# Performance work log

Measured on AMD Instinct MI355X. Metric: run time of the kernel, lower is better.

Reference implementation:

```python
import jax, jax.numpy as jnp
import numpy as np

HEADS = 16
LN_EPS = 1e-5

def setup_inputs() -> dict:
    key = jax.random.key(0)
    ks = jax.random.split(key, 8)
    B, S, NT = 4, 1024, 1024
    sc = 1.0 / np.sqrt(NT)
    return {
        "x": jax.random.normal(ks[0], (B, S, NT), dtype=jnp.float32),
        "Wq": jax.random.normal(ks[1], (NT, NT), dtype=jnp.float32) * sc,
        "bq": jax.random.normal(ks[2], (NT,), dtype=jnp.float32) * 0.02,
        "Wk": jax.random.normal(ks[3], (NT, NT), dtype=jnp.float32) * sc,
        "bk": jax.random.normal(ks[4], (NT,), dtype=jnp.float32) * 0.02,
        "Wv": jax.random.normal(ks[5], (NT, NT), dtype=jnp.float32) * sc,
        "bv": jax.random.normal(ks[6], (NT,), dtype=jnp.float32) * 0.02,
        "gamma": jnp.ones((NT,), dtype=jnp.float32),
        "beta": jnp.zeros((NT,), dtype=jnp.float32),
    }

def reference(x, Wq, bq, Wk, bk, Wv, bv, gamma, beta):
    B, S, nt = x.shape
    heads = HEADS
    dph = nt // heads
    # torch nn.Linear: y = x @ W.T + b
    q = x @ Wq.T + bq
    k = x @ Wk.T + bk
    v = x @ Wv.T + bv
    # torch .view(B*heads, -1, dph) is a row-major reshape (interleaved split)
    q = q.reshape(B * heads, -1, dph)
    k = k.reshape(B * heads, -1, dph)
    v = v.reshape(B * heads, -1, dph)
    # scaled scores; scale uses last dim of the score matrix (== seq len here)
    att = jnp.einsum('bid,bjd->bij', q, k)
    scale = att.shape[-1] ** (-0.5)
    att = jax.nn.softmax(jax.nn.relu(att * scale), axis=-1)
    # dropout in eval mode -> identity
    at_sum_sum = att.sum(axis=1).reshape(B, heads, -1)  # [B, heads, S]
    context = jnp.einsum('bij,bjd->bid', att, v).reshape(B, -1, nt)
    h = x + context
    mu = h.mean(axis=-1, keepdims=True)
    var = h.var(axis=-1, keepdims=True)
    out = (h - mu) * jax.lax.rsqrt(var + LN_EPS) * gamma + beta
    return out, at_sum_sum
```

## Files before the change

kernel.cpp:

```cpp
#include <hip/hip_runtime.h>
#include <hip/hip_bf16.h>
#include <cstdint>
#include <cstddef>


typedef short short8 __attribute__((ext_vector_type(8)));
typedef short short4v __attribute__((ext_vector_type(4)));
typedef float f32x4 __attribute__((ext_vector_type(4)));

#define MFMA32(a, b, c) __builtin_amdgcn_mfma_f32_16x16x32_bf16(a, b, c, 0, 0, 0)
#define MFMA16x16(a, b, c) __builtin_amdgcn_mfma_f32_16x16x16bf16_1k(a, b, c, 0, 0, 0)
#define ATT_SCALE 0.03125f

__device__ __forceinline__ short f2bf(float f) {
  union { float f; uint32_t u; } x; x.f = f;
  uint32_t u = x.u + 0x7fffu + ((x.u >> 16) & 1u);
  return (short)(u >> 16);
}

__device__ __forceinline__ uint32_t pk_bf16_trunc(float lo, float hi) {
  return __builtin_amdgcn_perm(__float_as_uint(hi), __float_as_uint(lo),
                               0x07060302u);
}

#define GLDS16(gp, lp)                                                        \
  __builtin_amdgcn_global_load_lds(                                           \
      (const __attribute__((address_space(1))) void*)(gp),                    \
      (__attribute__((address_space(3))) void*)(lp), 16, 0, 0)
#define GLDS4(gp, lp)                                                         \
  __builtin_amdgcn_global_load_lds(                                           \
      (const __attribute__((address_space(1))) void*)(gp),                    \
      (__attribute__((address_space(3))) void*)(lp), 4, 0, 0)

__global__ __launch_bounds__(256) void convert_kernel(
    const float* __restrict__ x, const float* __restrict__ wq,
    const float* __restrict__ wk, const float* __restrict__ wv,
    short* __restrict__ xb, short* __restrict__ wb,
    float* __restrict__ out2) {
  if (blockIdx.x >= 7168) {
    const int idx = (blockIdx.x - 7168) * 256 + threadIdx.x;
    *(f32x4*)(out2 + (size_t)idx * 4) = (f32x4){0.f, 0.f, 0.f, 0.f};
    return;
  }
  const long XN = 4L * 1024 * 1024, WN = 1024L * 1024;
  long e = (long)(blockIdx.x * blockDim.x + threadIdx.x) * 4;
  const float* src; short* dst;
  if (e < XN)               { src = x  + e;                dst = xb + e; }
  else if (e < XN + WN)     { src = wq + (e - XN);         dst = wb + (e - XN); }
  else if (e < XN + 2 * WN) { src = wk + (e - XN - WN);    dst = wb + (e - XN); }
  else                      { src = wv + (e - XN - 2*WN);  dst = wb + (e - XN); }
  f32x4 v = *(const f32x4*)src;
  short4v o;
  o[0] = f2bf(v[0]); o[1] = f2bf(v[1]); o[2] = f2bf(v[2]); o[3] = f2bf(v[3]);
  *(short4v*)dst = o;
}

__global__ __launch_bounds__(256, 3) void qkv_gemm(
    const short* __restrict__ xb, const short* __restrict__ wb,
    const float* __restrict__ bq, const float* __restrict__ bk,
    const float* __restrict__ bv, short* __restrict__ qb,
    short* __restrict__ kb, short* __restrict__ vtp) {
  __shared__ short As[128 * 64];
  __shared__ short Bs[128 * 64];
  const int tid = threadIdx.x;
  const int lane = tid & 63;
  const int lm = lane & 15, quad = lane >> 4;
  const int wave = tid >> 6, wy = wave >> 1, wx = wave & 1;
  const int f = blockIdx.x + (blockIdx.y << 3);
  const int r8 = f & 7, s = f >> 3;
  const int m0 = (((r8 >> 1) << 3) + (s & 7)) * 128;
  const int n0 = (((r8 & 1) << 2) + (s >> 3)) * 128;
  const int z = blockIdx.z;
  const short* w = wb + (size_t)z * (1024 * 1024);
  const float* bias = (z == 0) ? bq : (z == 1) ? bk : bv;
  const float scl = (z == 0) ? ATT_SCALE : 1.0f;

  const int srow = tid >> 3;
  const int schk = (tid & 7) ^ (srow & 7);
  const short* gA = xb + (size_t)(m0 + srow) * 1024 + schk * 8;
  const short* gB = w  + (size_t)(n0 + srow) * 1024 + schk * 8;
  short* lA = As + tid * 8;
  short* lB = Bs + tid * 8;

  f32x4 acc[4][4];
#pragma unroll
  for (int i = 0; i < 4; i++)
#pragma unroll
    for (int j = 0; j < 4; j++) acc[i][j] = (f32x4){0.f, 0.f, 0.f, 0.f};

  for (int k0 = 0; k0 < 1024; k0 += 64) {
#pragma unroll
    for (int q = 0; q < 4; q++) {
      GLDS16(gA + k0 + q * 32 * 1024, lA + q * 2048);
      GLDS16(gB + k0 + q * 32 * 1024, lB + q * 2048);
    }
    __syncthreads();
#pragma unroll
    for (int ks = 0; ks < 2; ks++) {
      const int ck = (((ks << 2) + quad) ^ (lm & 7)) * 8;
      short8 a[4], b[4];
#pragma unroll
      for (int t = 0; t < 4; t++) {
        a[t] = *(const short8*)(As + (wy * 64 + t * 16 + lm) * 64 + ck);
        b[t] = *(const short8*)(Bs + (wx * 64 + t * 16 + lm) * 64 + ck);
      }
#pragma unroll
      for (int mt = 0; mt < 4; mt++)
#pragma unroll
        for (int nt = 0; nt < 4; nt++)
          acc[mt][nt] = MFMA32(a[mt], b[nt], acc[mt][nt]);
    }
    __syncthreads();
  }
  if (z == 2) {
#pragma unroll
    for (int nt = 0; nt < 4; nt++) {
      const int n = n0 + wx * 64 + nt * 16 + lm;
      const float bn = bias[n];
      const size_t nbase = (size_t)((n >> 4) & 3) * 16384 +
                           (size_t)((((n >> 8) & 3) * 16 + (n & 15)) * 4 +
                                    ((n >> 6) & 3));
#pragma unroll
      for (int mt = 0; mt < 4; mt++) {
#pragma unroll
        for (int r = 0; r < 4; r++) {
          const int m = m0 + wy * 64 + mt * 16 + quad * 4 + r;
          vtp[(size_t)(m >> 6) * 65536 + nbase + (size_t)(m & 63) * 256] =
              f2bf(acc[mt][nt][r] + bn);
        }
      }
    }
  } else {
    short* out = (z == 0) ? qb : kb;
#pragma unroll
    for (int nt = 0; nt < 4; nt++) {
      const int n = n0 + wx * 64 + nt * 16 + lm;
      const float bn = bias[n];
#pragma unroll
      for (int mt = 0; mt < 4; mt++) {
        const int mb = m0 + wy * 64 + mt * 16 + quad * 4;
#pragma unroll
        for (int r = 0; r < 4; r++)
          out[(size_t)(mb + r) * 1024 + n] = f2bf((acc[mt][nt][r] + bn) * scl);
      }
    }
  }
}

__global__ __launch_bounds__(256, 2) void attn_kernel(
    const short* __restrict__ qb, const short* __restrict__ kb,
    const short* __restrict__ vtp, const float* __restrict__ x,
    const float* __restrict__ gamma, const float* __restrict__ beta,
    float* __restrict__ out1, float* __restrict__ rvW) {
  __shared__ short Ks[3][64 * 64];
  __shared__ short Vs[3][4 * 4 * 256];

  const int tid = threadIdx.x;
  const int lane = tid & 63, wave = tid >> 6;
  const int lm = lane & 15, quad = lane >> 4;
  const int bid = blockIdx.x;
  const int h = ((bid >> 6) << 3) + (bid & 7);
  const int bb = (bid >> 3) & 7;
  const short* Qh = qb + (size_t)h * 65536;
  const short* Kh = kb + (size_t)h * 65536;
  const short* Vp = vtp + (size_t)h * 65536;
  const int i0 = bb * 128 + wave * 32;

  const short8 qA0 = *(const short8*)(Qh + (size_t)(i0 + lm) * 64 + quad * 8);
  const short8 qA1 = *(const short8*)(Qh + (size_t)(i0 + lm) * 64 + 32 + quad * 8);
  const short8 qB0 = *(const short8*)(Qh + (size_t)(i0 + 16 + lm) * 64 + quad * 8);
  const short8 qB1 = *(const short8*)(Qh + (size_t)(i0 + 16 + lm) * 64 + 32 + quad * 8);

  const int c0 = tid, c1 = tid + 256;
  const short* gK0 = Kh + (size_t)(c0 >> 3) * 64 + ((c0 & 7) ^ ((c0 >> 3) & 7)) * 8;
  const short* gK1 = Kh + (size_t)(c1 >> 3) * 64 + ((c1 & 7) ^ ((c1 >> 3) & 7)) * 8;
  const short* gV0 = Vp + (c0 >> 7) * 16384 + ((c0 >> 5) & 3) * 256 + (c0 & 31) * 8;
  const short* gV1 = Vp + (c1 >> 7) * 16384 + ((c1 >> 5) & 3) * 256 + (c1 & 31) * 8;
  const int lK0 = c0 * 8, lK1 = c1 * 8;

#define ATTN_STAGE(c, buf)                                                    \
  do {                                                                        \
    const int ko_ = ((c) & 15) * 4096, vo_ = ((c) & 15) * 1024;               \
    GLDS16(gK0 + ko_, &Ks[buf][0] + lK0);                                     \
    GLDS16(gK1 + ko_, &Ks[buf][0] + lK1);                                     \
    GLDS16(gV0 + vo_, &Vs[buf][0] + lK0);                                     \
    GLDS16(gV1 + vo_, &Vs[buf][0] + lK1);                                     \
  } while (0)

  f32x4 accA[4], accB[4];
#pragma unroll
  for (int t = 0; t < 4; t++) {
    accA[t] = (f32x4){0.f, 0.f, 0.f, 0.f};
    accB[t] = (f32x4){0.f, 0.f, 0.f, 0.f};
  }
  float dsA[4] = {0.f, 0.f, 0.f, 0.f};
  float dsB[4] = {0.f, 0.f, 0.f, 0.f};

  const int swz0 = (quad ^ (lm & 7)) * 8;
  const int swz1 = ((quad + 4) ^ (lm & 7)) * 8;

  ATTN_STAGE(0, 0);
  ATTN_STAGE(1, 1);

  for (int ch = 0; ch < 16; ch++) {
    const int b = ch % 3, bs = (ch + 2) % 3;
    asm volatile("s_waitcnt vmcnt(4)" ::: "memory");
    __builtin_amdgcn_s_barrier();
    __builtin_amdgcn_s_setprio(1);
#pragma unroll
    for (int jj = 0; jj < 4; jj++) {
      const short* krow = &Ks[b][(jj * 16 + lm) * 64];
      const short8 kf0 = *(const short8*)(krow + swz0);
      const short8 kf1 = *(const short8*)(krow + swz1);
      f32x4 zA = {0.f, 0.f, 0.f, 0.f};
      zA = MFMA32(kf0, qA0, zA);
      zA = MFMA32(kf1, qA1, zA);
      f32x4 zB = {0.f, 0.f, 0.f, 0.f};
      zB = MFMA32(kf0, qB0, zB);
      zB = MFMA32(kf1, qB1, zB);
      float pA[4], pB[4];
#pragma unroll
      for (int r = 0; r < 4; r++) {
        pA[r] = __expf(fmaxf(zA[r], 0.f));
        dsA[r] += pA[r];
        pB[r] = __expf(fmaxf(zB[r], 0.f));
        dsB[r] += pB[r];
      }
      union { uint32_t u[2]; short4v s; } puA, puB;
      puA.u[0] = pk_bf16_trunc(pA[0], pA[1]);
      puA.u[1] = pk_bf16_trunc(pA[2], pA[3]);
      puB.u[0] = pk_bf16_trunc(pB[0], pB[1]);
      puB.u[1] = pk_bf16_trunc(pB[2], pB[3]);
      const short* vbase = &Vs[b][jj * 256 + lane * 4];
#pragma unroll
      for (int dt = 0; dt < 4; dt++) {
        const short4v vtf = *(const short4v*)(vbase + dt * 1024);
        accA[dt] = MFMA16x16(vtf, puA.s, accA[dt]);
        accB[dt] = MFMA16x16(vtf, puB.s, accB[dt]);
      }
    }
    __builtin_amdgcn_s_setprio(0);
    if (ch < 15) ATTN_STAGE(ch + 2, bs);
  }
  asm volatile("s_waitcnt vmcnt(0)" ::: "memory");

  float tA = (dsA[0] + dsA[1]) + (dsA[2] + dsA[3]);
  tA += __shfl_xor(tA, 16);
  tA += __shfl_xor(tA, 32);
  float tB = (dsB[0] + dsB[1]) + (dsB[2] + dsB[3]);
  tB += __shfl_xor(tB, 16);
  tB += __shfl_xor(tB, 32);
  const float rvA = 1.f / tA;
  const float rvB = 1.f / tB;
  if (lane < 16) {
    rvW[h * 1024 + i0 + lm] = rvA;
    rvW[h * 1024 + i0 + 16 + lm] = rvB;
  }

  const int mA = h * 64 + bb * 8 + wave * 2;
  const int nb = lm * 64 + quad * 4;
#pragma unroll
  for (int tile = 0; tile < 2; tile++) {
    const int m = mA + tile;
    const f32x4* accT = tile ? accB : accA;
    const float rv = tile ? rvB : rvA;
    const float* xr = x + (size_t)m * 1024;
    float hv[4][4], s1 = 0.f, s2 = 0.f;
#pragma unroll
    for (int dt = 0; dt < 4; dt++) {
      f32x4 xv = *(const f32x4*)(xr + nb + dt * 16);
#pragma unroll
      for (int r = 0; r < 4; r++) {
        const float v = xv[r] + accT[dt][r] * rv;
        hv[dt][r] = v; s1 += v; s2 += v * v;
      }
    }
#pragma unroll
    for (int mk = 1; mk < 64; mk <<= 1) {
      s1 += __shfl_xor(s1, mk);
      s2 += __shfl_xor(s2, mk);
    }
    const float mu = s1 * (1.f / 1024.f);
    const float var = s2 * (1.f / 1024.f) - mu * mu;
    const float rstd = rsqrtf(var + 1e-5f);
    float* orow = out1 + (size_t)m * 1024;
#pragma unroll
    for (int dt = 0; dt < 4; dt++) {
      f32x4 gv = *(const f32x4*)(gamma + nb + dt * 16);
      f32x4 bv2 = *(const f32x4*)(beta + nb + dt * 16);
      f32x4 ov;
#pragma unroll
      for (int r = 0; r < 4; r++)
        ov[r] = (hv[dt][r] - mu) * rstd * gv[r] + bv2[r];
      *(f32x4*)(orow + nb + dt * 16) = ov;
    }
  }
}

__global__ __launch_bounds__(256, 4) void colsum_kernel(
    const short* __restrict__ qb, const short* __restrict__ kb,
    const float* __restrict__ rvW, float* __restrict__ out2) {
  __shared__ short Qs[3][64 * 64];
  __shared__ float rvS[3][64];

  const int tid = threadIdx.x;
  const int lane = tid & 63, wave = tid >> 6;
  const int lm = lane & 15, quad = lane >> 4;
  const int bid = blockIdx.x;
  const int h = ((bid >> 7) << 3) + (bid & 7);
  const int jb = (bid >> 3) & 7;
  const int ih = (bid >> 6) & 1;
  const int cb = ih * 8;
  const int j0 = jb * 128 + wave * 32;
  const short* Qh = qb + (size_t)h * 65536;
  const short* Kh = kb + (size_t)h * 65536;
  const float* rvh = rvW + h * 1024;

  const short* krA = Kh + (size_t)(j0 + lm) * 64 + quad * 8;
  const short8 kA0 = *(const short8*)krA;
  const short8 kA1 = *(const short8*)(krA + 32);
  const short* krB = Kh + (size_t)(j0 + 16 + lm) * 64 + quad * 8;
  const short8 kB0 = *(const short8*)krB;
  const short8 kB1 = *(const short8*)(krB + 32);

  const int c0 = tid, c1 = tid + 256;
  const short* gQ0 = Qh + (size_t)(c0 >> 3) * 64 + ((c0 & 7) ^ ((c0 >> 3) & 7)) * 8;
  const short* gQ1 = Qh + (size_t)(c1 >> 3) * 64 + ((c1 & 7) ^ ((c1 >> 3) & 7)) * 8;
  const int lQ0 = c0 * 8, lQ1 = c1 * 8;

#define CS_STAGE(c, buf)                                                      \
  do {                                                                        \
    const int qo_ = ((c) & 15) * 4096;                                        \
    GLDS16(gQ0 + qo_, &Qs[buf][0] + lQ0);                                     \
    GLDS16(gQ1 + qo_, &Qs[buf][0] + lQ1);                                     \
    GLDS4(rvh + ((c) & 15) * 64 + lane, &rvS[buf][0]);                        \
  } while (0)

  const int swz0 = (quad ^ (lm & 7)) * 8;
  const int swz1 = ((quad + 4) ^ (lm & 7)) * 8;

  f32x4 csA = {0.f, 0.f, 0.f, 0.f};
  f32x4 csB = {0.f, 0.f, 0.f, 0.f};

  CS_STAGE(cb, 0);
  CS_STAGE(cb + 1, 1);

  for (int ch = 0; ch < 8; ch++) {
    const int b = ch % 3, bs = (ch + 2) % 3;
    asm volatile("s_waitcnt vmcnt(3)" ::: "memory");
    __builtin_amdgcn_s_barrier();
    __builtin_amdgcn_s_setprio(1);
#pragma unroll
    for (int ii = 0; ii < 4; ii++) {
      const short* qrow = &Qs[b][(ii * 16 + lm) * 64];
      const short8 qf0 = *(const short8*)(qrow + swz0);
      const short8 qf1 = *(const short8*)(qrow + swz1);
      f32x4 zA = {0.f, 0.f, 0.f, 0.f};
      zA = MFMA32(kA0, qf0, zA);
      zA = MFMA32(kA1, qf1, zA);
      f32x4 zB = {0.f, 0.f, 0.f, 0.f};
      zB = MFMA32(kB0, qf0, zB);
      zB = MFMA32(kB1, qf1, zB);
      const float rvv = rvS[b][ii * 16 + lm];
#pragma unroll
      for (int r = 0; r < 4; r++) {
        csA[r] += __expf(fmaxf(zA[r], 0.f)) * rvv;
        csB[r] += __expf(fmaxf(zB[r], 0.f)) * rvv;
      }
    }
    __builtin_amdgcn_s_setprio(0);
    if (ch < 7) CS_STAGE((cb + ch + 2) & 15, bs);
  }
  asm volatile("s_waitcnt vmcnt(0)" ::: "memory");

#pragma unroll
  for (int mk = 1; mk < 16; mk <<= 1)
#pragma unroll
    for (int r = 0; r < 4; r++) {
      csA[r] += __shfl_xor(csA[r], mk);
      csB[r] += __shfl_xor(csB[r], mk);
    }
  if (lm == 0) {
    float* pA = out2 + h * 1024 + j0 + quad * 4;
    float* pB = pA + 16;
#pragma unroll
    for (int r = 0; r < 4; r++) {
      atomicAdd(pA + r, csA[r]);
      atomicAdd(pB + r, csB[r]);
    }
  }
}

extern "C" void kernel_launch(void* const* d_in, const int* in_sizes, int n_in,
                              void* d_out, int out_size, void* d_ws, size_t ws_size,
                              hipStream_t stream) {
  const float* x  = (const float*)d_in[0];
  const float* Wq = (const float*)d_in[1];
  const float* bq = (const float*)d_in[2];
  const float* Wk = (const float*)d_in[3];
  const float* bk = (const float*)d_in[4];
  const float* Wv = (const float*)d_in[5];
  const float* bv = (const float*)d_in[6];
  const float* gamma = (const float*)d_in[7];
  const float* beta  = (const float*)d_in[8];

  float* out1 = (float*)d_out;
  float* out2 = out1 + 4L * 1024 * 1024;

  short* xb = (short*)d_ws;
  short* wb = xb + 4L * 1024 * 1024;
  short* qb = wb + 3L * 1024 * 1024;
  short* kb = qb + 4L * 1024 * 1024;
  short* vtp = kb + 4L * 1024 * 1024;
  float* rvW = (float*)wb;

  convert_kernel<<<7232, 256, 0, stream>>>(x, Wq, Wk, Wv, xb, wb, out2);
  qkv_gemm<<<dim3(8, 32, 3), 256, 0, stream>>>(xb, wb, bq, bk, bv, qb, kb, vtp);
  attn_kernel<<<512, 256, 0, stream>>>(qb, kb, vtp, x, gamma, beta, out1, rvW);
  colsum_kernel<<<1024, 256, 0, stream>>>(qb, kb, rvW, out2);
}
```

Measured before the change: 165.3 us.

## Fold log2e into Q scale, read V and colsum Q directly from global

Folds log2(e) into the Q projection scale so both softmax kernels can call the hardware exp2 instruction instead of __expf. In the attention kernel, V fragments are no longer staged through LDS; each lane loads them straight from global memory. In the colsum kernel, the LDS staging and barriers for Q and the row values are removed in favour of direct global loads. The aim is to cut LDS traffic, barriers and the extra multiply in exp, at the risk of exposing global load latency inside the MFMA loop.

```diff
diff --git a/kernel.cpp b/kernel.cpp
--- a/kernel.cpp
+++ b/kernel.cpp
@@ -10,7 +10,7 @@
 
 #define MFMA32(a, b, c) __builtin_amdgcn_mfma_f32_16x16x32_bf16(a, b, c, 0, 0, 0)
 #define MFMA16x16(a, b, c) __builtin_amdgcn_mfma_f32_16x16x16bf16_1k(a, b, c, 0, 0, 0)
-#define ATT_SCALE 0.03125f
+#define QSCALE 0.045084220027780106f
 
 __device__ __forceinline__ short f2bf(float f) {
   union { float f; uint32_t u; } x; x.f = f;
@@ -27,10 +27,6 @@
   __builtin_amdgcn_global_load_lds(                                           \
       (const __attribute__((address_space(1))) void*)(gp),                    \
       (__attribute__((address_space(3))) void*)(lp), 16, 0, 0)
-#define GLDS4(gp, lp)                                                         \
-  __builtin_amdgcn_global_load_lds(                                           \
-      (const __attribute__((address_space(1))) void*)(gp),                    \
-      (__attribute__((address_space(3))) void*)(lp), 4, 0, 0)
 
 __global__ __launch_bounds__(256) void convert_kernel(
     const float* __restrict__ x, const float* __restrict__ wq,
@@ -73,7 +69,7 @@
   const int z = blockIdx.z;
   const short* w = wb + (size_t)z * (1024 * 1024);
   const float* bias = (z == 0) ? bq : (z == 1) ? bk : bv;
-  const float scl = (z == 0) ? ATT_SCALE : 1.0f;
+  const float scl = (z == 0) ? QSCALE : 1.0f;
 
   const int srow = tid >> 3;
   const int schk = (tid & 7) ^ (srow & 7);
@@ -153,7 +149,6 @@
     const float* __restrict__ gamma, const float* __restrict__ beta,
     float* __restrict__ out1, float* __restrict__ rvW) {
   __shared__ short Ks[3][64 * 64];
-  __shared__ short Vs[3][4 * 4 * 256];
 
   const int tid = threadIdx.x;
   const int lane = tid & 63, wave = tid >> 6;
@@ -174,17 +169,14 @@
   const int c0 = tid, c1 = tid + 256;
   const short* gK0 = Kh + (size_t)(c0 >> 3) * 64 + ((c0 & 7) ^ ((c0 >> 3) & 7)) * 8;
   const short* gK1 = Kh + (size_t)(c1 >> 3) * 64 + ((c1 & 7) ^ ((c1 >> 3) & 7)) * 8;
-  const short* gV0 = Vp + (c0 >> 7) * 16384 + ((c0 >> 5) & 3) * 256 + (c0 & 31) * 8;
-  const short* gV1 = Vp + (c1 >> 7) * 16384 + ((c1 >> 5) & 3) * 256 + (c1 & 31) * 8;
   const int lK0 = c0 * 8, lK1 = c1 * 8;
+  const short* vl = Vp + lane * 4;
 
 #define ATTN_STAGE(c, buf)                                                    \
   do {                                                                        \
-    const int ko_ = ((c) & 15) * 4096, vo_ = ((c) & 15) * 1024;               \
+    const int ko_ = ((c) & 15) * 4096;                                        \
     GLDS16(gK0 + ko_, &Ks[buf][0] + lK0);                                     \
     GLDS16(gK1 + ko_, &Ks[buf][0] + lK1);                                     \
-    GLDS16(gV0 + vo_, &Vs[buf][0] + lK0);                                     \
-    GLDS16(gV1 + vo_, &Vs[buf][0] + lK1);                                     \
   } while (0)
 
   f32x4 accA[4], accB[4];
@@ -204,9 +196,10 @@
 
   for (int ch = 0; ch < 16; ch++) {
     const int b = ch % 3, bs = (ch + 2) % 3;
-    asm volatile("s_waitcnt vmcnt(4)" ::: "memory");
+    asm volatile("s_waitcnt vmcnt(2)" ::: "memory");
     __builtin_amdgcn_s_barrier();
     __builtin_amdgcn_s_setprio(1);
+    const short* vc = vl + ch * 1024;
 #pragma unroll
     for (int jj = 0; jj < 4; jj++) {
       const short* krow = &Ks[b][(jj * 16 + lm) * 64];
@@ -221,9 +214,9 @@
       float pA[4], pB[4];
 #pragma unroll
       for (int r = 0; r < 4; r++) {
-        pA[r] = __expf(fmaxf(zA[r], 0.f));
+        pA[r] = __builtin_amdgcn_exp2f(fmaxf(zA[r], 0.f));
         dsA[r] += pA[r];
-        pB[r] = __expf(fmaxf(zB[r], 0.f));
+        pB[r] = __builtin_amdgcn_exp2f(fmaxf(zB[r], 0.f));
         dsB[r] += pB[r];
       }
       union { uint32_t u[2]; short4v s; } puA, puB;
@@ -231,10 +224,10 @@
       puA.u[1] = pk_bf16_trunc(pA[2], pA[3]);
       puB.u[0] = pk_bf16_trunc(pB[0], pB[1]);
       puB.u[1] = pk_bf16_trunc(pB[2], pB[3]);
-      const short* vbase = &Vs[b][jj * 256 + lane * 4];
+      const short* vj = vc + jj * 256;
 #pragma unroll
       for (int dt = 0; dt < 4; dt++) {
-        const short4v vtf = *(const short4v*)(vbase + dt * 1024);
+        const short4v vtf = *(const short4v*)(vj + dt * 16384);
         accA[dt] = MFMA16x16(vtf, puA.s, accA[dt]);
         accB[dt] = MFMA16x16(vtf, puB.s, accB[dt]);
       }
@@ -300,9 +293,6 @@
 __global__ __launch_bounds__(256, 4) void colsum_kernel(
     const short* __restrict__ qb, const short* __restrict__ kb,
     const float* __restrict__ rvW, float* __restrict__ out2) {
-  __shared__ short Qs[3][64 * 64];
-  __shared__ float rvS[3][64];
-
   const int tid = threadIdx.x;
   const int lane = tid & 63, wave = tid >> 6;
   const int lm = lane & 15, quad = lane >> 4;
@@ -310,11 +300,10 @@
   const int h = ((bid >> 7) << 3) + (bid & 7);
   const int jb = (bid >> 3) & 7;
   const int ih = (bid >> 6) & 1;
-  const int cb = ih * 8;
   const int j0 = jb * 128 + wave * 32;
-  const short* Qh = qb + (size_t)h * 65536;
+  const short* Qh = qb + (size_t)h * 65536 + (size_t)ih * 32768;
   const short* Kh = kb + (size_t)h * 65536;
-  const float* rvh = rvW + h * 1024;
+  const float* rvh = rvW + h * 1024 + ih * 512;
 
   const short* krA = Kh + (size_t)(j0 + lm) * 64 + quad * 8;
   const short8 kA0 = *(const short8*)krA;
@@ -323,55 +312,33 @@
   const short8 kB0 = *(const short8*)krB;
   const short8 kB1 = *(const short8*)(krB + 32);
 
-  const int c0 = tid, c1 = tid + 256;
-  const short* gQ0 = Qh + (size_t)(c0 >> 3) * 64 + ((c0 & 7) ^ ((c0 >> 3) & 7)) * 8;
-  const short* gQ1 = Qh + (size_t)(c1 >> 3) * 64 + ((c1 & 7) ^ ((c1 >> 3) & 7)) * 8;
-  const int lQ0 = c0 * 8, lQ1 = c1 * 8;
-
-#define CS_STAGE(c, buf)                                                      \
-  do {                                                                        \
-    const int qo_ = ((c) & 15) * 4096;                                        \
-    GLDS16(gQ0 + qo_, &Qs[buf][0] + lQ0);                                     \
-    GLDS16(gQ1 + qo_, &Qs[buf][0] + lQ1);                                     \
-    GLDS4(rvh + ((c) & 15) * 64 + lane, &rvS[buf][0]);                        \
-  } while (0)
-
-  const int swz0 = (quad ^ (lm & 7)) * 8;
-  const int swz1 = ((quad + 4) ^ (lm & 7)) * 8;
-
   f32x4 csA = {0.f, 0.f, 0.f, 0.f};
   f32x4 csB = {0.f, 0.f, 0.f, 0.f};
 
-  CS_STAGE(cb, 0);
-  CS_STAGE(cb + 1, 1);
-
   for (int ch = 0; ch < 8; ch++) {
-    const int b = ch % 3, bs = (ch + 2) % 3;
-    asm volatile("s_waitcnt vmcnt(3)" ::: "memory");
-    __builtin_amdgcn_s_barrier();
+    const short* qc = Qh + ch * 4096 + (size_t)lm * 64 + quad * 8;
+    const float* rvc = rvh + ch * 64 + lm;
     __builtin_amdgcn_s_setprio(1);
 #pragma unroll
     for (int ii = 0; ii < 4; ii++) {
-      const short* qrow = &Qs[b][(ii * 16 + lm) * 64];
-      const short8 qf0 = *(const short8*)(qrow + swz0);
-      const short8 qf1 = *(const short8*)(qrow + swz1);
+      const short* qrow = qc + ii * 1024;
+      const short8 qf0 = *(const short8*)qrow;
+      const short8 qf1 = *(const short8*)(qrow + 32);
       f32x4 zA = {0.f, 0.f, 0.f, 0.f};
       zA = MFMA32(kA0, qf0, zA);
       zA = MFMA32(kA1, qf1, zA);
       f32x4 zB = {0.f, 0.f, 0.f, 0.f};
       zB = MFMA32(kB0, qf0, zB);
       zB = MFMA32(kB1, qf1, zB);
-      const float rvv = rvS[b][ii * 16 + lm];
+      const float rvv = rvc[ii * 16];
 #pragma unroll
       for (int r = 0; r < 4; r++) {
-        csA[r] += __expf(fmaxf(zA[r], 0.f)) * rvv;
-        csB[r] += __expf(fmaxf(zB[r], 0.f)) * rvv;
+        csA[r] += __builtin_amdgcn_exp2f(fmaxf(zA[r], 0.f)) * rvv;
+        csB[r] += __builtin_amdgcn_exp2f(fmaxf(zB[r], 0.f)) * rvv;
       }
     }
     __builtin_amdgcn_s_setprio(0);
-    if (ch < 7) CS_STAGE((cb + ch + 2) & 15, bs);
-  }
-  asm volatile("s_waitcnt vmcnt(0)" ::: "memory");
+  }
 
 #pragma unroll
   for (int mk = 1; mk < 16; mk <<= 1)
```

Result: slower. 181.3 us (+9.7%).

## Halve attention rows per block, double grid, fold log2e into Q scale

Applied to the files above, without the earlier changes.

The attention kernel now gives each wave 16 query rows instead of 32 and launches twice as many blocks. LDS staging drops from triple to double buffering, and launch bounds rise to 4 blocks per CU for more occupancy. The Q projection scale is multiplied by log2(e) so both attention and colsum can use the native exp2 instead of __expf. The cost is twice the K/V traffic per query row and a full vmcnt(0) wait each chunk, which removes some load/compute overlap.

```diff
diff --git a/kernel.cpp b/kernel.cpp
--- a/kernel.cpp
+++ b/kernel.cpp
@@ -10,7 +10,7 @@
 
 #define MFMA32(a, b, c) __builtin_amdgcn_mfma_f32_16x16x32_bf16(a, b, c, 0, 0, 0)
 #define MFMA16x16(a, b, c) __builtin_amdgcn_mfma_f32_16x16x16bf16_1k(a, b, c, 0, 0, 0)
-#define ATT_SCALE 0.03125f
+#define QSCALE 0.045084220027780106f
 
 __device__ __forceinline__ short f2bf(float f) {
   union { float f; uint32_t u; } x; x.f = f;
@@ -73,7 +73,7 @@
   const int z = blockIdx.z;
   const short* w = wb + (size_t)z * (1024 * 1024);
   const float* bias = (z == 0) ? bq : (z == 1) ? bk : bv;
-  const float scl = (z == 0) ? ATT_SCALE : 1.0f;
+  const float scl = (z == 0) ? QSCALE : 1.0f;
 
   const int srow = tid >> 3;
   const int schk = (tid & 7) ^ (srow & 7);
@@ -147,29 +147,27 @@
   }
 }
 
-__global__ __launch_bounds__(256, 2) void attn_kernel(
+__global__ __launch_bounds__(256, 4) void attn_kernel(
     const short* __restrict__ qb, const short* __restrict__ kb,
     const short* __restrict__ vtp, const float* __restrict__ x,
     const float* __restrict__ gamma, const float* __restrict__ beta,
     float* __restrict__ out1, float* __restrict__ rvW) {
-  __shared__ short Ks[3][64 * 64];
-  __shared__ short Vs[3][4 * 4 * 256];
+  __shared__ short Ks[2][64 * 64];
+  __shared__ short Vs[2][4 * 4 * 256];
 
   const int tid = threadIdx.x;
   const int lane = tid & 63, wave = tid >> 6;
   const int lm = lane & 15, quad = lane >> 4;
   const int bid = blockIdx.x;
-  const int h = ((bid >> 6) << 3) + (bid & 7);
-  const int bb = (bid >> 3) & 7;
+  const int h = ((bid >> 7) << 3) + (bid & 7);
+  const int blk = (bid >> 3) & 15;
   const short* Qh = qb + (size_t)h * 65536;
   const short* Kh = kb + (size_t)h * 65536;
   const short* Vp = vtp + (size_t)h * 65536;
-  const int i0 = bb * 128 + wave * 32;
+  const int i0 = blk * 64 + wave * 16;
 
   const short8 qA0 = *(const short8*)(Qh + (size_t)(i0 + lm) * 64 + quad * 8);
   const short8 qA1 = *(const short8*)(Qh + (size_t)(i0 + lm) * 64 + 32 + quad * 8);
-  const short8 qB0 = *(const short8*)(Qh + (size_t)(i0 + 16 + lm) * 64 + quad * 8);
-  const short8 qB1 = *(const short8*)(Qh + (size_t)(i0 + 16 + lm) * 64 + 32 + quad * 8);
 
   const int c0 = tid, c1 = tid + 256;
   const short* gK0 = Kh + (size_t)(c0 >> 3) * 64 + ((c0 & 7) ^ ((c0 >> 3) & 7)) * 8;
@@ -180,32 +178,28 @@
 
 #define ATTN_STAGE(c, buf)                                                    \
   do {                                                                        \
-    const int ko_ = ((c) & 15) * 4096, vo_ = ((c) & 15) * 1024;               \
+    const int ko_ = (c) * 4096, vo_ = (c) * 1024;                             \
     GLDS16(gK0 + ko_, &Ks[buf][0] + lK0);                                     \
     GLDS16(gK1 + ko_, &Ks[buf][0] + lK1);                                     \
     GLDS16(gV0 + vo_, &Vs[buf][0] + lK0);                                     \
     GLDS16(gV1 + vo_, &Vs[buf][0] + lK1);                                     \
   } while (0)
 
-  f32x4 accA[4], accB[4];
-#pragma unroll
-  for (int t = 0; t < 4; t++) {
-    accA[t] = (f32x4){0.f, 0.f, 0.f, 0.f};
-    accB[t] = (f32x4){0.f, 0.f, 0.f, 0.f};
-  }
+  f32x4 accA[4];
+#pragma unroll
+  for (int t = 0; t < 4; t++) accA[t] = (f32x4){0.f, 0.f, 0.f, 0.f};
   float dsA[4] = {0.f, 0.f, 0.f, 0.f};
-  float dsB[4] = {0.f, 0.f, 0.f, 0.f};
 
   const int swz0 = (quad ^ (lm & 7)) * 8;
   const int swz1 = ((quad + 4) ^ (lm & 7)) * 8;
 
   ATTN_STAGE(0, 0);
-  ATTN_STAGE(1, 1);
 
   for (int ch = 0; ch < 16; ch++) {
-    const int b = ch % 3, bs = (ch + 2) % 3;
-    asm volatile("s_waitcnt vmcnt(4)" ::: "memory");
+    const int b = ch & 1;
+    asm volatile("s_waitcnt vmcnt(0)" ::: "memory");
     __builtin_amdgcn_s_barrier();
+    if (ch < 15) ATTN_STAGE(ch + 1, b ^ 1);
     __builtin_amdgcn_s_setprio(1);
 #pragma unroll
     for (int jj = 0; jj < 4; jj++) {
@@ -215,85 +209,62 @@
       f32x4 zA = {0.f, 0.f, 0.f, 0.f};
       zA = MFMA32(kf0, qA0, zA);
       zA = MFMA32(kf1, qA1, zA);
-      f32x4 zB = {0.f, 0.f, 0.f, 0.f};
-      zB = MFMA32(kf0, qB0, zB);
-      zB = MFMA32(kf1, qB1, zB);
-      float pA[4], pB[4];
+      float pA[4];
 #pragma unroll
       for (int r = 0; r < 4; r++) {
-        pA[r] = __expf(fmaxf(zA[r], 0.f));
+        pA[r] = __builtin_amdgcn_exp2f(fmaxf(zA[r], 0.f));
         dsA[r] += pA[r];
-        pB[r] = __expf(fmaxf(zB[r], 0.f));
-        dsB[r] += pB[r];
-      }
-      union { uint32_t u[2]; short4v s; } puA, puB;
+      }
+      union { uint32_t u[2]; short4v s; } puA;
       puA.u[0] = pk_bf16_trunc(pA[0], pA[1]);
       puA.u[1] = pk_bf16_trunc(pA[2], pA[3]);
-      puB.u[0] = pk_bf16_trunc(pB[0], pB[1]);
-      puB.u[1] = pk_bf16_trunc(pB[2], pB[3]);
       const short* vbase = &Vs[b][jj * 256 + lane * 4];
 #pragma unroll
       for (int dt = 0; dt < 4; dt++) {
         const short4v vtf = *(const short4v*)(vbase + dt * 1024);
         accA[dt] = MFMA16x16(vtf, puA.s, accA[dt]);
-        accB[dt] = MFMA16x16(vtf, puB.s, accB[dt]);
       }
     }
     __builtin_amdgcn_s_setprio(0);
-    if (ch < 15) ATTN_STAGE(ch + 2, bs);
-  }
-  asm volatile("s_waitcnt vmcnt(0)" ::: "memory");
+  }
 
   float tA = (dsA[0] + dsA[1]) + (dsA[2] + dsA[3]);
   tA += __shfl_xor(tA, 16);
   tA += __shfl_xor(tA, 32);
-  float tB = (dsB[0] + dsB[1]) + (dsB[2] + dsB[3]);
-  tB += __shfl_xor(tB, 16);
-  tB += __shfl_xor(tB, 32);
   const float rvA = 1.f / tA;
-  const float rvB = 1.f / tB;
-  if (lane < 16) {
-    rvW[h * 1024 + i0 + lm] = rvA;
-    rvW[h * 1024 + i0 + 16 + lm] = rvB;
-  }
-
-  const int mA = h * 64 + bb * 8 + wave * 2;
+  if (lane < 16) rvW[h * 1024 + i0 + lm] = rvA;
+
+  const int m = h * 64 + blk * 4 + wave;
   const int nb = lm * 64 + quad * 4;
-#pragma unroll
-  for (int tile = 0; tile < 2; tile++) {
-    const int m = mA + tile;
-    const f32x4* accT = tile ? accB : accA;
-    const float rv = tile ? rvB : rvA;
-    const float* xr = x + (size_t)m * 1024;
-    float hv[4][4], s1 = 0.f, s2 = 0.f;
-#pragma unroll
-    for (int dt = 0; dt < 4; dt++) {
-      f32x4 xv = *(const f32x4*)(xr + nb + dt * 16);
-#pragma unroll
-      for (int r = 0; r < 4; r++) {
-        const float v = xv[r] + accT[dt][r] * rv;
-        hv[dt][r] = v; s1 += v; s2 += v * v;
-      }
-    }
-#pragma unroll
-    for (int mk = 1; mk < 64; mk <<= 1) {
-      s1 += __shfl_xor(s1, mk);
-      s2 += __shfl_xor(s2, mk);
-    }
-    const float mu = s1 * (1.f / 1024.f);
-    const float var = s2 * (1.f / 1024.f) - mu * mu;
-    const float rstd = rsqrtf(var + 1e-5f);
-    float* orow = out1 + (size_t)m * 1024;
-#pragma unroll
-    for (int dt = 0; dt < 4; dt++) {
-      f32x4 gv = *(const f32x4*)(gamma + nb + dt * 16);
-      f32x4 bv2 = *(const f32x4*)(beta + nb + dt * 16);
-      f32x4 ov;
-#pragma unroll
-      for (int r = 0; r < 4; r++)
-        ov[r] = (hv[dt][r] - mu) * rstd * gv[r] + bv2[r];
-      *(f32x4*)(orow + nb + dt * 16) = ov;
-    }
+  const float* xr = x + (size_t)m * 1024;
+  float hv[4][4], s1 = 0.f, s2 = 0.f;
+#pragma unroll
+  for (int dt = 0; dt < 4; dt++) {
+    f32x4 xv = *(const f32x4*)(xr + nb + dt * 16);
+#pragma unroll
+    for (int r = 0; r < 4; r++) {
+      const float v = xv[r] + accA[dt][r] * rvA;
+      hv[dt][r] = v; s1 += v; s2 += v * v;
+    }
+  }
+#pragma unroll
+  for (int mk = 1; mk < 64; mk <<= 1) {
+    s1 += __shfl_xor(s1, mk);
+    s2 += __shfl_xor(s2, mk);
+  }
+  const float mu = s1 * (1.f / 1024.f);
+  const float var = s2 * (1.f / 1024.f) - mu * mu;
+  const float rstd = rsqrtf(var + 1e-5f);
+  float* orow = out1 + (size_t)m * 1024;
+#pragma unroll
+  for (int dt = 0; dt < 4; dt++) {
+    f32x4 gv = *(const f32x4*)(gamma + nb + dt * 16);
+    f32x4 bv2 = *(const f32x4*)(beta + nb + dt * 16);
+    f32x4 ov;
+#pragma unroll
+    for (int r = 0; r < 4; r++)
+      ov[r] = (hv[dt][r] - mu) * rstd * gv[r] + bv2[r];
+    *(f32x4*)(orow + nb + dt * 16) = ov;
   }
 }
 
@@ -364,8 +335,8 @@
       const float rvv = rvS[b][ii * 16 + lm];
 #pragma unroll
       for (int r = 0; r < 4; r++) {
-        csA[r] += __expf(fmaxf(zA[r], 0.f)) * rvv;
-        csB[r] += __expf(fmaxf(zB[r], 0.f)) * rvv;
+        csA[r] += __builtin_amdgcn_exp2f(fmaxf(zA[r], 0.f)) * rvv;
+        csB[r] += __builtin_amdgcn_exp2f(fmaxf(zB[r], 0.f)) * rvv;
       }
     }
     __builtin_amdgcn_s_setprio(0);
@@ -416,6 +387,6 @@
 
   convert_kernel<<<7232, 256, 0, stream>>>(x, Wq, Wk, Wv, xb, wb, out2);
   qkv_gemm<<<dim3(8, 32, 3), 256, 0, stream>>>(xb, wb, bq, bk, bv, qb, kb, vtp);
-  attn_kernel<<<512, 256, 0, stream>>>(qb, kb, vtp, x, gamma, beta, out1, rvW);
+  attn_kernel<<<1024, 256, 0, stream>>>(qb, kb, vtp, x, gamma, beta, out1, rvW);
   colsum_kernel<<<1024, 256, 0, stream>>>(qb, kb, rvW, out2);
 }
```

Result: slower. 169.7 us (+2.7%).
